# Performance work log

Hardware: AMD Instinct MI355X
Metric: run time of the kernel (lower is better)

## Reference

```python
import jax, jax.numpy as jnp
import numpy as np

K = 20           # neighbors
ALPHA = 1.0      # clustering alpha
BN_EPS = 1e-5
NEG_SLOPE = 0.2


def knn_idx(x, k):
    # x: (B, C, N) -> idx (B, N, k) of k nearest neighbors by squared L2
    xx = jnp.sum(x * x, axis=1)                      # (B, N)
    inner = jnp.einsum('bcn,bcm->bnm', x, x)         # (B, N, N)
    pd = -xx[:, :, None] + 2.0 * inner - xx[:, None, :]  # negative sq dist
    return jax.lax.top_k(pd, k)[1]


def graph_feature(x, k):
    # x: (B, C, N) -> (B, 2C, N, k): concat(neighbor - center, center)
    xt = jnp.transpose(x, (0, 2, 1))                 # (B, N, C)
    idx = knn_idx(x, k)                              # (B, N, k)
    feat = jax.vmap(lambda f, i: f[i])(xt, idx)      # (B, N, k, C)
    center = jnp.broadcast_to(xt[:, :, None, :], feat.shape)
    out = jnp.concatenate([feat - center, center], axis=-1)
    return jnp.transpose(out, (0, 3, 1, 2))


def batchnorm(x, g, b, axes):
    # training-mode BN: batch statistics over `axes`, channel axis = 1
    m = jnp.mean(x, axes, keepdims=True)
    v = jnp.var(x, axes, keepdims=True)
    shape = [1] * x.ndim
    shape[1] = x.shape[1]
    return (x - m) / jnp.sqrt(v + BN_EPS) * g.reshape(shape) + b.reshape(shape)


def conv_block2d(x, w, g, b):
    # 1x1 Conv2d (no bias) + BN2d + LeakyReLU; x (B,Cin,N,k), w (Cout,Cin)
    y = jnp.einsum('oc,bcnk->bonk', w, x)
    return jax.nn.leaky_relu(batchnorm(y, g, b, (0, 2, 3)), NEG_SLOPE)


def setup_inputs() -> dict:
    key = jax.random.key(0)
    ks = jax.random.split(key, 16)
    B, C, N = 4, 3, 2048
    d = {
        'x1': jax.random.normal(ks[0], (B, C, N), jnp.float32),
        'x2': jax.random.normal(ks[1], (B, C, N), jnp.float32),
        'w1': jax.random.normal(ks[2], (64, 6), jnp.float32) * 0.1,
        'g1': jnp.ones((64,), jnp.float32), 'b1': jnp.zeros((64,), jnp.float32),
        'w2': jax.random.normal(ks[3], (64, 128), jnp.float32) * 0.1,
        'g2': jnp.ones((64,), jnp.float32), 'b2': jnp.zeros((64,), jnp.float32),
        'w3': jax.random.normal(ks[4], (128, 128), jnp.float32) * 0.1,
        'g3': jnp.ones((128,), jnp.float32), 'b3': jnp.zeros((128,), jnp.float32),
        'w4': jax.random.normal(ks[5], (256, 256), jnp.float32) * 0.1,
        'g4': jnp.ones((256,), jnp.float32), 'b4': jnp.zeros((256,), jnp.float32),
        'w5': jax.random.normal(ks[6], (1024, 512), jnp.float32) * 0.05,
        'g5': jnp.ones((1024,), jnp.float32), 'b5': jnp.zeros((1024,), jnp.float32),
        'lw1': jax.random.normal(ks[7], (256, 2048), jnp.float32) * 0.02,
        'lb1': jnp.zeros((256,), jnp.float32),
        'lw2': jax.random.normal(ks[8], (64, 256), jnp.float32) * 0.05,
        'lb2': jnp.zeros((64,), jnp.float32),
        'lw3': jax.random.normal(ks[9], (10, 64), jnp.float32) * 0.1,
        'lb3': jnp.zeros((10,), jnp.float32),
        'cw': jax.random.normal(ks[10], (800, 10), jnp.float32) * 0.1,
    }
    return d


def reference(x1, x2, w1, g1, b1, w2, g2, b2, w3, g3, b3, w4, g4, b4,
              w5, g5, b5, lw1, lb1, lw2, lb2, lw3, lb3, cw):

    def single(x):
        h = conv_block2d(graph_feature(x, K), w1, g1, b1)
        f1 = h.max(axis=-1)                            # (B,64,N)
        h = conv_block2d(graph_feature(f1, K), w2, g2, b2)
        f2 = h.max(axis=-1)                            # (B,64,N)
        h = conv_block2d(graph_feature(f2, K), w3, g3, b3)
        f3 = h.max(axis=-1)                            # (B,128,N)
        h = conv_block2d(graph_feature(f3, K), w4, g4, b4)
        f4 = h.max(axis=-1)                            # (B,256,N)
        h = jnp.concatenate([f1, f2, f3, f4], axis=1)  # (B,512,N)
        h = jnp.einsum('oc,bcn->bon', w5, h)           # 1x1 Conv1d
        h = jax.nn.leaky_relu(batchnorm(h, g5, b5, (0, 2)), NEG_SLOPE)
        z = jnp.concatenate([h.max(axis=-1), h.mean(axis=-1)], axis=1)  # (B,2048)
        z = z @ lw1.T + lb1
        z = z @ lw2.T + lb2
        e = z @ lw3.T + lb3                            # (B,10)
        diff = e[:, None, :] - cw                      # (B,800,10)
        x_dis = jnp.sum(diff * diff, axis=2)           # (B,800)
        q = (1.0 + x_dis / ALPHA) ** (-(ALPHA + 1.0) / 2.0)
        q = q / jnp.sum(q, axis=1, keepdims=True)
        return q, e, x_dis

    q1, e1, xd1 = single(x1)
    q2, e2, xd2 = single(x2)
    d = e1 - e2 + 1e-6  # torch F.pairwise_distance eps
    sim = jnp.sqrt(jnp.sum(d * d, axis=1))
    return (sim, q1, q2, e1, e2, xd1)
```

## Files before the change

kernel.cpp:

```cpp
#include <hip/hip_runtime.h>
#include <math.h>

#define BB 4
#define NN 2048
#define KK 20
#define NEG 0.2f

#define QOFF0 4
#define QOFF1 3204
#define EOFF0 6404
#define EOFF1 6444
#define XDOFF 6484

typedef unsigned short u16;
typedef unsigned int u32;
typedef __attribute__((ext_vector_type(8))) short s16x8;
typedef __attribute__((ext_vector_type(16))) float f32x16;
typedef __attribute__((ext_vector_type(8))) u16 u16x8;

__global__ __launch_bounds__(256) void transpose_x_kernel(
    const float* __restrict__ x, float* __restrict__ fnc, float* __restrict__ xx)
{
    int gid = blockIdx.x * 256 + threadIdx.x;
    int b = gid >> 11, n = gid & 2047;
    float s = 0.f;
#pragma unroll
    for (int c = 0; c < 3; ++c) {
        float v = x[((size_t)b * 3 + c) * NN + n];
        fnc[(size_t)gid * 3 + c] = v;
        s += v * v;
    }
    xx[gid] = s;
}

__global__ __launch_bounds__(256) void norms_kernel(
    const float* __restrict__ h512, int choff, int C, float* __restrict__ xx)
{
    int gid = blockIdx.x * 256 + threadIdx.x;
    const float* p = h512 + (size_t)gid * 512 + choff;
    float s = 0.f;
    for (int c = 0; c < C; ++c) { float v = p[c]; s += v * v; }
    xx[gid] = s;
}

#define NINFV -3.4e38f

template<int CTRL>
__device__ __forceinline__ void dmax2(float& a1, float& a2)
{
    int b1i = __builtin_amdgcn_update_dpp(
        __float_as_int(a1), __float_as_int(a1), CTRL, 0xf, 0xf, false);
    int b2i = __builtin_amdgcn_update_dpp(
        __float_as_int(a2), __float_as_int(a2), CTRL, 0xf, 0xf, false);
    float b1 = __int_as_float(b1i), b2 = __int_as_float(b2i);
    float n1 = fmaxf(a1, b1);
    float n2 = fmaxf(fminf(a1, b1), fmaxf(a2, b2));
    a1 = n1; a2 = n2;
}

template<int C>
__global__ __launch_bounds__(512, 4) void knn_kernel(
    const float* __restrict__ fcn,
    const float* __restrict__ fnc,
    int ncs, int choff,
    const float* __restrict__ xx, int* __restrict__ idxout)
{
    __shared__ float sbuf[8][NN];
    int tid = threadIdx.x;
    int bid = blockIdx.x;
    int b   = bid & 3;
    int n0  = (((bid >> 3) << 1) | ((bid >> 2) & 1)) * 8;

    const float* fb = fcn + (size_t)b * C * NN;
    const float* xb = xx + b * NN;
    const float* cbase = fnc + (size_t)(b * NN + n0) * ncs + choff;

    float a0[8], a1[8], a2[8], a3[8];
#pragma unroll
    for (int r = 0; r < 8; ++r) { a0[r] = 0.f; a1[r] = 0.f; a2[r] = 0.f; a3[r] = 0.f; }

    const float* fp = fb + 4 * tid;

    if constexpr (C % 4 == 0) {
        float4 buf[4];
#pragma unroll
        for (int q = 0; q < 4; ++q) buf[q] = *(const float4*)(fp + (size_t)q * NN);
        for (int cg = 0; cg < C; cg += 4) {
            float4 nxt[4];
            if (cg + 4 < C) {
#pragma unroll
                for (int q = 0; q < 4; ++q)
                    nxt[q] = *(const float4*)(fp + (size_t)(cg + 4 + q) * NN);
            } else {
#pragma unroll
                for (int q = 0; q < 4; ++q) nxt[q] = buf[q];
            }
            float4 cv[8];
#pragma unroll
            for (int r = 0; r < 8; ++r)
                cv[r] = *(const float4*)(cbase + (size_t)r * ncs + cg);
#pragma unroll
            for (int r = 0; r < 8; ++r) {
                a0[r] += cv[r].x * buf[0].x; a1[r] += cv[r].x * buf[0].y;
                a2[r] += cv[r].x * buf[0].z; a3[r] += cv[r].x * buf[0].w;
                a0[r] += cv[r].y * buf[1].x; a1[r] += cv[r].y * buf[1].y;
                a2[r] += cv[r].y * buf[1].z; a3[r] += cv[r].y * buf[1].w;
                a0[r] += cv[r].z * buf[2].x; a1[r] += cv[r].z * buf[2].y;
                a2[r] += cv[r].z * buf[2].z; a3[r] += cv[r].z * buf[2].w;
                a0[r] += cv[r].w * buf[3].x; a1[r] += cv[r].w * buf[3].y;
                a2[r] += cv[r].w * buf[3].z; a3[r] += cv[r].w * buf[3].w;
            }
#pragma unroll
            for (int q = 0; q < 4; ++q) buf[q] = nxt[q];
        }
    } else {
        for (int c = 0; c < C; ++c) {
            float cr[8];
#pragma unroll
            for (int r = 0; r < 8; ++r) cr[r] = cbase[(size_t)r * ncs + c];
            float4 v = *(const float4*)(fp + (size_t)c * NN);
#pragma unroll
            for (int r = 0; r < 8; ++r) {
                a0[r] += cr[r] * v.x; a1[r] += cr[r] * v.y;
                a2[r] += cr[r] * v.z; a3[r] += cr[r] * v.w;
            }
        }
    }
    {
        float4 xm = *(const float4*)(xb + 4 * tid);
#pragma unroll
        for (int r = 0; r < 8; ++r) {
            float4 sv = {2.f * a0[r] - xm.x, 2.f * a1[r] - xm.y,
                         2.f * a2[r] - xm.z, 2.f * a3[r] - xm.w};
            *(float4*)&sbuf[r][4 * tid] = sv;
        }
    }
    __syncthreads();

    int w = tid >> 6, lane = tid & 63;
    float* sb = sbuf[w];
    int p = n0 + w;
    int* op = idxout + (size_t)(b * NN + p) * KK;

    if (lane == 0) op[0] = p;
    if (lane == (p & 63)) sb[p] = NINFV;

    float v1 = NINFV, v2 = NINFV, v3 = NINFV, v4 = NINFV;
    int j1 = -1, j2 = -1, j3 = -1, j4 = -1;
#pragma unroll
    for (int j = 0; j < 32; ++j) {
        float vv = sb[lane + (j << 6)];
        if (vv > v1) { v4 = v3; j4 = j3; v3 = v2; j3 = j2; v2 = v1; j2 = j1; v1 = vv; j1 = j; }
        else if (vv > v2) { v4 = v3; j4 = j3; v3 = v2; j3 = j2; v2 = vv; j2 = j; }
        else if (vv > v3) { v4 = v3; j4 = j3; v3 = vv; j3 = j; }
        else if (vv > v4) { v4 = vv; j4 = j; }
    }

    unsigned consumed = 0u;

    for (int it = 1; it < KK; it += 2) {
        float r1 = v1, r2 = v2;
        dmax2<0x111>(r1, r2);
        dmax2<0x112>(r1, r2);
        dmax2<0x114>(r1, r2);
        dmax2<0x118>(r1, r2);
        dmax2<0x142>(r1, r2);
        dmax2<0x143>(r1, r2);
        float m1 = __int_as_float(
            __builtin_amdgcn_readlane(__float_as_int(r1), 63));
        float m2 = __int_as_float(
            __builtin_amdgcn_readlane(__float_as_int(r2), 63));
        unsigned long long k1 = __ballot(v1 == m1);
        if (lane == __ffsll(k1) - 1) {
            op[it] = lane + (j1 << 6);
            consumed |= 1u << j1;
            v1 = v2; j1 = j2; v2 = v3; j2 = j3; v3 = v4; j3 = j4;
            v4 = NINFV; j4 = -1;
        }
        if (it + 1 < KK) {
            unsigned long long k2 = __ballot(v1 == m2);
            if (lane == __ffsll(k2) - 1) {
                op[it + 1] = lane + (j1 << 6);
                consumed |= 1u << j1;
                v1 = v2; j1 = j2; v2 = v3; j2 = j3; v3 = v4; j3 = j4;
                v4 = NINFV; j4 = -1;
            }
        }
        if (__any(v2 == NINFV)) {
            if (v2 == NINFV) {
                v1 = NINFV; v2 = NINFV; v3 = NINFV; v4 = NINFV;
                j1 = -1; j2 = -1; j3 = -1; j4 = -1;
#pragma unroll
                for (int j = 0; j < 32; ++j) {
                    if (!(consumed & (1u << j))) {
                        float vv = sb[lane + (j << 6)];
                        if (vv > v1) { v4 = v3; j4 = j3; v3 = v2; j3 = j2; v2 = v1; j2 = j1; v1 = vv; j1 = j; }
                        else if (vv > v2) { v4 = v3; j4 = j3; v3 = v2; j3 = j2; v2 = vv; j2 = j; }
                        else if (vv > v3) { v4 = v3; j4 = j3; v3 = vv; j3 = j; }
                        else if (vv > v4) { v4 = vv; j4 = j; }
                    }
                }
            }
        }
    }
}

template<int C, int COUT>
__global__ __launch_bounds__(256) void gemm_gh_kernel(
    const float* __restrict__ fnc, int ncs, int choff,
    const float* __restrict__ W,
    float* __restrict__ G, float* __restrict__ H)
{
    constexpr int GROUPS = 256 / COUT;
    constexpr int RPT = 8 / GROUPS;
    __shared__ float Fs[8][C];
    int tid = threadIdx.x;
    int row0 = blockIdx.x * 8;
    for (int i = tid; i < 8 * C; i += 256) {
        int r = i / C, c = i % C;
        Fs[r][c] = fnc[(size_t)(row0 + r) * ncs + choff + c];
    }
    __syncthreads();
    int o = tid % COUT;
    int r0 = (tid / COUT) * RPT;
    float g[RPT], h[RPT];
#pragma unroll
    for (int r = 0; r < RPT; ++r) { g[r] = 0.f; h[r] = 0.f; }
    const float* wr = W + (size_t)o * 2 * C;
    for (int c = 0; c < C; ++c) {
        float w1 = wr[c], wd = wr[C + c] - w1;
#pragma unroll
        for (int r = 0; r < RPT; ++r) {
            float f = Fs[r0 + r][c];
            g[r] += f * w1; h[r] += f * wd;
        }
    }
#pragma unroll
    for (int r = 0; r < RPT; ++r) {
        size_t rr = (size_t)(row0 + r0 + r) * COUT + o;
        G[rr] = g[r]; H[rr] = h[r];
    }
}

template<int COUT>
__global__ __launch_bounds__(256) void gather_kernel(
    const float* __restrict__ G, const float* __restrict__ H,
    const int* __restrict__ idx,
    float* __restrict__ ymax, float* __restrict__ ymin,
    float* __restrict__ psum, float* __restrict__ psumsq)
{
    constexpr int RPI = 256 / COUT;
    constexpr int NITER = 16 / RPI;
    int tid = threadIdx.x;
    int o = tid % COUT;
    int rsub = tid / COUT;
    int row0 = blockIdx.x * 16;
    float s = 0.f, s2 = 0.f;
    for (int it = 0; it < NITER; ++it) {
        int r = row0 + it * RPI + rsub;
        int b = r >> 11;
        float h = H[(size_t)r * COUT + o];
        const int* ip = idx + (size_t)r * KK;
        float mx = -3.4e38f, mn = 3.4e38f;
#pragma unroll
        for (int j = 0; j < KK; ++j) {
            int m = ip[j];
            float g = G[((size_t)(b << 11) + m) * COUT + o];
            float y = g + h;
            mx = fmaxf(mx, y); mn = fminf(mn, y);
            s += y; s2 += y * y;
        }
        ymax[(size_t)r * COUT + o] = mx;
        ymin[(size_t)r * COUT + o] = mn;
    }
    __shared__ float ls[256], ls2[256];
    ls[tid] = s; ls2[tid] = s2;
    __syncthreads();
    for (int st = 128; st >= COUT; st >>= 1) {
        if (tid < st) { ls[tid] += ls[tid + st]; ls2[tid] += ls2[tid + st]; }
        __syncthreads();
    }
    if (tid < COUT) {
        psum[(size_t)blockIdx.x * COUT + tid]   = ls[tid];
        psumsq[(size_t)blockIdx.x * COUT + tid] = ls2[tid];
    }
}

__global__ __launch_bounds__(256) void bnscale_kernel(
    const float* __restrict__ psum, const float* __restrict__ psumsq,
    int nblk, int cout, float cnt,
    const float* __restrict__ gw, const float* __restrict__ bw,
    float* __restrict__ ss)
{
    int o = blockIdx.x;
    int t = threadIdx.x;
    float s = 0.f, s2 = 0.f;
    for (int i = t; i < nblk; i += 256) {
        s  += psum[(size_t)i * cout + o];
        s2 += psumsq[(size_t)i * cout + o];
    }
    __shared__ float ls[256], ls2[256];
    ls[t] = s; ls2[t] = s2;
    __syncthreads();
    for (int st = 128; st > 0; st >>= 1) {
        if (t < st) { ls[t] += ls[t + st]; ls2[t] += ls2[t + st]; }
        __syncthreads();
    }
    if (t == 0) {
        float m = ls[0] / cnt;
        float v = ls2[0] / cnt - m * m;
        float sc = gw[o] / sqrtf(v + 1e-5f);
        float sh = bw[o] - m * sc;
        ss[o * 2] = sc; ss[o * 2 + 1] = sh;
    }
}

__global__ __launch_bounds__(256) void apply_kernel(
    const float* __restrict__ ymax, const float* __restrict__ ymin,
    const float* __restrict__ ss, int coutShift, int choff,
    float* __restrict__ h512)
{
    size_t gid = (size_t)blockIdx.x * 256 + threadIdx.x;
    int o = (int)(gid & ((1u << coutShift) - 1));
    size_t r = gid >> coutShift;
    float sc = ss[o * 2], sh = ss[o * 2 + 1];
    float v = (sc >= 0.f) ? ymax[gid] : ymin[gid];
    float a = sc * v + sh;
    float act = (a > 0.f) ? a : NEG * a;
    h512[r * 512 + choff + o] = act;
}

template<int CO>
__global__ __launch_bounds__(256) void apply_t_kernel(
    const float* __restrict__ ymax, const float* __restrict__ ymin,
    const float* __restrict__ ss, int choff,
    float* __restrict__ h512, float* __restrict__ fcn)
{
    constexpr int TILES_O = CO >> 6;
    __shared__ float tile[64][65];
    int tr = blockIdx.x / TILES_O;
    int to = blockIdx.x % TILES_O;
    int r0 = tr * 64, o0 = to * 64;
    int t = threadIdx.x;
    int lr = t >> 6;
    int lo = t & 63;
    int o = o0 + lo;
    float sc = ss[o * 2], sh = ss[o * 2 + 1];
#pragma unroll
    for (int rr = 0; rr < 64; rr += 4) {
        int r = r0 + rr + lr;
        size_t gid = (size_t)r * CO + o;
        float v = (sc >= 0.f) ? ymax[gid] : ymin[gid];
        float a = sc * v + sh;
        float act = (a > 0.f) ? a : NEG * a;
        h512[(size_t)r * 512 + choff + o] = act;
        tile[rr + lr][lo] = act;
    }
    __syncthreads();
    int b = r0 >> 11;
    int n0 = r0 & 2047;
#pragma unroll
    for (int oo = 0; oo < 64; oo += 4) {
        fcn[((size_t)(b * CO + o0 + oo + lr)) * NN + n0 + lo] = tile[lo][oo + lr];
    }
}

__device__ __forceinline__ u16 f2bf(float x) {
    u32 u = __float_as_uint(x);
    u += 0x7FFFu + ((u >> 16) & 1u);
    return (u16)(u >> 16);
}

__global__ __launch_bounds__(256) void tobf16_kernel(
    const float* __restrict__ A, const float* __restrict__ Bm,
    u16* __restrict__ Ah, u16* __restrict__ Al,
    u16* __restrict__ Bh, u16* __restrict__ Bl)
{
    int gid = blockIdx.x * 256 + threadIdx.x;
    const float* src; u16 *dh, *dl; size_t off;
    if (gid < 524288) { src = A;  dh = Ah; dl = Al; off = (size_t)gid * 8; }
    else             { src = Bm; dh = Bh; dl = Bl; off = (size_t)(gid - 524288) * 8; }
    float4 v0 = *(const float4*)(src + off);
    float4 v1 = *(const float4*)(src + off + 4);
    float x[8] = {v0.x, v0.y, v0.z, v0.w, v1.x, v1.y, v1.z, v1.w};
    u16x8 h, l;
#pragma unroll
    for (int j = 0; j < 8; ++j) {
        u16 hb = f2bf(x[j]);
        h[j] = hb;
        l[j] = f2bf(x[j] - __uint_as_float((u32)hb << 16));
    }
    *(u16x8*)(dh + off) = h;
    *(u16x8*)(dl + off) = l;
}

__device__ __forceinline__ void gload_lds16(const void* g, void* l) {
    __builtin_amdgcn_global_load_lds(
        (const __attribute__((address_space(1))) void*)g,
        (__attribute__((address_space(3))) void*)l, 16, 0, 0);
}

__global__ __launch_bounds__(256) void gemm5_mfma_kernel(
    const u16* __restrict__ Ah, const u16* __restrict__ Al,
    const u16* __restrict__ Bh, const u16* __restrict__ Bl,
    float* __restrict__ Y, float* __restrict__ psum, float* __restrict__ psumsq)
{
    __shared__ u16 As[2][128][64];
    __shared__ u16 Bs[2][128][64];
    __shared__ float scs[4][128];
    __shared__ float sqs[4][128];

    int tid = threadIdx.x;
    int bm = blockIdx.x & 63, bn = blockIdx.x >> 6;
    int row0 = bm * 128, col0 = bn * 128;
    int w = tid >> 6, lane = tid & 63;
    int wr = w >> 1, wc = w & 1;

    int isB = w >> 1, plane = w & 1;
    int srow = lane >> 3;
    int kch  = (lane & 7) ^ srow;
    const u16* gbase = isB ? (plane ? Bl : Bh) : (plane ? Al : Ah);
    int rc0 = isB ? col0 : row0;
    const u16* gsrc0 = gbase + (size_t)(rc0 + srow) * 512 + kch * 8;
    u16* lds0 = (isB ? &Bs[0][0][0] : &As[0][0][0]) + plane * 8192;

    f32x16 acc[2][2];
#pragma unroll
    for (int i = 0; i < 2; ++i)
#pragma unroll
        for (int j = 0; j < 2; ++j)
#pragma unroll
            for (int r = 0; r < 16; ++r) acc[i][j][r] = 0.f;

    int ln = lane & 31, l5 = lane >> 5;
    const u16* Afb = &As[0][0][0] + (size_t)(wr * 64 + ln) * 64;
    const u16* Bfb = &Bs[0][0][0] + (size_t)(wc * 64 + ln) * 64;

    for (int k0 = 0; k0 < 512; k0 += 64) {
#pragma unroll
        for (int cc = 0; cc < 16; ++cc)
            gload_lds16(gsrc0 + (size_t)cc * 4096 + k0, lds0 + cc * 512);
        __syncthreads();

#pragma unroll
        for (int ks = 0; ks < 4; ++ks) {
            int pos = ((ks * 2 + l5) ^ (ln & 7)) * 8;
            s16x8 ah0 = *(const s16x8*)(Afb + pos);
            s16x8 ah1 = *(const s16x8*)(Afb + 2048 + pos);
            s16x8 al0 = *(const s16x8*)(Afb + 8192 + pos);
            s16x8 al1 = *(const s16x8*)(Afb + 8192 + 2048 + pos);
#pragma unroll
            for (int j = 0; j < 2; ++j) {
                s16x8 bh = *(const s16x8*)(Bfb + j * 2048 + pos);
                s16x8 bl = *(const s16x8*)(Bfb + 8192 + j * 2048 + pos);
                acc[0][j] = __builtin_amdgcn_mfma_f32_32x32x16_bf16(ah0, bh, acc[0][j], 0, 0, 0);
                acc[1][j] = __builtin_amdgcn_mfma_f32_32x32x16_bf16(ah1, bh, acc[1][j], 0, 0, 0);
                acc[0][j] = __builtin_amdgcn_mfma_f32_32x32x16_bf16(al0, bh, acc[0][j], 0, 0, 0);
                acc[1][j] = __builtin_amdgcn_mfma_f32_32x32x16_bf16(al1, bh, acc[1][j], 0, 0, 0);
                acc[0][j] = __builtin_amdgcn_mfma_f32_32x32x16_bf16(ah0, bl, acc[0][j], 0, 0, 0);
                acc[1][j] = __builtin_amdgcn_mfma_f32_32x32x16_bf16(ah1, bl, acc[1][j], 0, 0, 0);
            }
        }
        __syncthreads();
    }

#pragma unroll
    for (int i = 0; i < 2; ++i)
#pragma unroll
        for (int reg = 0; reg < 16; ++reg) {
            int row = row0 + wr * 64 + i * 32 + l5 * 4 + (reg >> 2) * 8 + (reg & 3);
            float* yp = Y + (size_t)row * 1024 + col0 + wc * 64 + ln;
            yp[0]  = acc[i][0][reg];
            yp[32] = acc[i][1][reg];
        }

#pragma unroll
// ... 137 lines not shown
#pragma unroll
        for (int i = 0; i < 10; ++i) { float d = es[b][i] - cwr[i]; xd += d * d; }
        qs[p] = 1.0f / (1.0f + xd);
        if (which == 0) out[XDOFF + p] = xd;
    }
    __syncthreads();
    if (t < 4) {
        float s = 0.f;
        for (int j = 0; j < 800; ++j) s += qs[t * 800 + j];
        dnm[t] = s;
    }
    __syncthreads();
    int qoff = (which == 0) ? QOFF0 : QOFF1;
    for (int p = t; p < 3200; p += 1024) out[qoff + p] = qs[p] / dnm[p / 800];
}

__global__ void sim_kernel(const float* __restrict__ e_store, float* __restrict__ out)
{
    int t = threadIdx.x;
    if (t < 4) {
        float s = 0.f;
        for (int i = 0; i < 10; ++i) {
            float d = e_store[t * 10 + i] - e_store[40 + t * 10 + i] + 1e-6f;
            s += d * d;
        }
        out[t] = sqrtf(s);
    }
}

extern "C" void kernel_launch(void* const* d_in, const int* in_sizes, int n_in,
                              void* d_out, int out_size, void* d_ws, size_t ws_size,
                              hipStream_t stream)
{
    const float* x1  = (const float*)d_in[0];
    const float* x2  = (const float*)d_in[1];
    const float* w1  = (const float*)d_in[2];
    const float* g1  = (const float*)d_in[3];
    const float* b1  = (const float*)d_in[4];
    const float* w2  = (const float*)d_in[5];
    const float* g2  = (const float*)d_in[6];
    const float* b2  = (const float*)d_in[7];
    const float* w3  = (const float*)d_in[8];
    const float* g3  = (const float*)d_in[9];
    const float* b3  = (const float*)d_in[10];
    const float* w4  = (const float*)d_in[11];
    const float* g4  = (const float*)d_in[12];
    const float* b4  = (const float*)d_in[13];
    const float* w5  = (const float*)d_in[14];
    const float* g5  = (const float*)d_in[15];
    const float* b5  = (const float*)d_in[16];
    const float* lw1 = (const float*)d_in[17];
    const float* lb1 = (const float*)d_in[18];
    const float* lw2 = (const float*)d_in[19];
    const float* lb2 = (const float*)d_in[20];
    const float* lw3 = (const float*)d_in[21];
    const float* lb3 = (const float*)d_in[22];
    const float* cw  = (const float*)d_in[23];
    float* out = (float*)d_out;

    float* ws   = (float*)d_ws;
    float* h512 = ws;
    float* G    = h512 + 4194304;
    float* Hb   = G + 2097152;
    float* ymax = Hb + 2097152;
    float* ymin = ymax + 2097152;
    float* y5   = G;
    float* fcn  = ymin + 2097152;
    float* fnc1 = fcn + 1048576;
    float* xx   = fnc1 + 32768;
    float* psum = xx + 8192;
    float* psq  = psum + 131072;
    float* ss   = psq + 131072;
    float* p5s  = ss + 2048;
    float* p5q  = p5s + 262144;
    float* ss5  = p5q + 262144;
    float* z    = ss5 + 2048;
    float* z1   = z + 8192;
    float* est  = z1 + 1024;
    int*   idx  = (int*)(est + 128);
    u16*   Ahs  = (u16*)(idx + BB * NN * KK);
    u16*   Als  = Ahs + 4194304;
    u16*   Bhs  = Als + 4194304;
    u16*   Bls  = Bhs + 524288;

    for (int which = 0; which < 2; ++which) {
        const float* xin = which ? x2 : x1;
        transpose_x_kernel<<<32, 256, 0, stream>>>(xin, fnc1, xx);
        knn_kernel<3><<<1024, 512, 0, stream>>>(xin, fnc1, 3, 0, xx, idx);
        gemm_gh_kernel<3, 64><<<1024, 256, 0, stream>>>(fnc1, 3, 0, w1, G, Hb);
        gather_kernel<64><<<512, 256, 0, stream>>>(G, Hb, idx, ymax, ymin, psum, psq);
        bnscale_kernel<<<64, 256, 0, stream>>>(psum, psq, 512, 64, 163840.f, g1, b1, ss);
        apply_t_kernel<64><<<128, 256, 0, stream>>>(ymax, ymin, ss, 0, h512, fcn);
        norms_kernel<<<32, 256, 0, stream>>>(h512, 0, 64, xx);
        knn_kernel<64><<<1024, 512, 0, stream>>>(fcn, h512, 512, 0, xx, idx);
        gemm_gh_kernel<64, 64><<<1024, 256, 0, stream>>>(h512, 512, 0, w2, G, Hb);
        gather_kernel<64><<<512, 256, 0, stream>>>(G, Hb, idx, ymax, ymin, psum, psq);
        bnscale_kernel<<<64, 256, 0, stream>>>(psum, psq, 512, 64, 163840.f, g2, b2, ss);
        apply_t_kernel<64><<<128, 256, 0, stream>>>(ymax, ymin, ss, 64, h512, fcn);
        norms_kernel<<<32, 256, 0, stream>>>(h512, 64, 64, xx);
        knn_kernel<64><<<1024, 512, 0, stream>>>(fcn, h512, 512, 64, xx, idx);
        gemm_gh_kernel<64, 128><<<1024, 256, 0, stream>>>(h512, 512, 64, w3, G, Hb);
        gather_kernel<128><<<512, 256, 0, stream>>>(G, Hb, idx, ymax, ymin, psum, psq);
        bnscale_kernel<<<128, 256, 0, stream>>>(psum, psq, 512, 128, 163840.f, g3, b3, ss);
        apply_t_kernel<128><<<256, 256, 0, stream>>>(ymax, ymin, ss, 128, h512, fcn);
        norms_kernel<<<32, 256, 0, stream>>>(h512, 128, 128, xx);
        knn_kernel<128><<<1024, 512, 0, stream>>>(fcn, h512, 512, 128, xx, idx);
        gemm_gh_kernel<128, 256><<<1024, 256, 0, stream>>>(h512, 512, 128, w4, G, Hb);
        gather_kernel<256><<<512, 256, 0, stream>>>(G, Hb, idx, ymax, ymin, psum, psq);
        bnscale_kernel<<<256, 256, 0, stream>>>(psum, psq, 512, 256, 163840.f, g4, b4, ss);
        apply_kernel<<<8192, 256, 0, stream>>>(ymax, ymin, ss, 8, 256, h512);
        tobf16_kernel<<<2304, 256, 0, stream>>>(h512, w5, Ahs, Als, Bhs, Bls);
        gemm5_mfma_kernel<<<512, 256, 0, stream>>>(Ahs, Als, Bhs, Bls, y5, p5s, p5q);
        bnscale_kernel<<<1024, 256, 0, stream>>>(p5s, p5q, 64, 1024, 8192.f, g5, b5, ss5);
        pool_part_kernel<<<256, 256, 0, stream>>>(y5, ss5, p5s, p5q);
        pool_comb_kernel<<<4, 256, 0, stream>>>(p5s, p5q, z);
        gemv1_kernel<<<256, 64, 0, stream>>>(z, lw1, lb1, z1);
        head2_kernel<<<1, 1024, 0, stream>>>(z1, lw2, lb2, lw3, lb3, cw, out, est, which);
    }
    sim_kernel<<<1, 64, 0, stream>>>(est, out);
}
```

Baseline: 1.170 ms.

## Compute kNN distance matrix with split-bf16 MFMA and fuse bf16 conversion into apply

Replaces the FP32 CUDA-core inner-product loop in the kNN kernel with 16x16x32 bf16 MFMA using a hi/lo split (three products) to approximate FP32 accuracy, processing 16 query points per 1024-thread block. The bf16 hi/lo copies of activations are now written directly by the apply kernels and by the input transpose (zero-padded to 32 channels), and the standalone tobf16 pass for the activations is removed. The weight conversion is hoisted out of the per-input loop. This adds extra stores in the apply kernels and risks small distance errors that could change neighbor selection on near ties.

Measured after the change: 1.239 ms. 1.06x slower.

```diff
diff --git a/kernel.cpp b/kernel.cpp
--- a/kernel.cpp
+++ b/kernel.cpp
@@ -15,22 +15,45 @@
 typedef unsigned short u16;
 typedef unsigned int u32;
 typedef __attribute__((ext_vector_type(8))) short s16x8;
+typedef __attribute__((ext_vector_type(4))) float f32x4;
 typedef __attribute__((ext_vector_type(16))) float f32x16;
 typedef __attribute__((ext_vector_type(8))) u16 u16x8;
 
+__device__ __forceinline__ u16 f2bf(float x) {
+    u32 u = __float_as_uint(x);
+    u += 0x7FFFu + ((u >> 16) & 1u);
+    return (u16)(u >> 16);
+}
+
 __global__ __launch_bounds__(256) void transpose_x_kernel(
-    const float* __restrict__ x, float* __restrict__ fnc, float* __restrict__ xx)
+    const float* __restrict__ x, float* __restrict__ fnc, float* __restrict__ xx,
+    u16* __restrict__ fh, u16* __restrict__ fl)
 {
     int gid = blockIdx.x * 256 + threadIdx.x;
     int b = gid >> 11, n = gid & 2047;
     float s = 0.f;
+    float v[3];
 #pragma unroll
     for (int c = 0; c < 3; ++c) {
-        float v = x[((size_t)b * 3 + c) * NN + n];
-        fnc[(size_t)gid * 3 + c] = v;
-        s += v * v;
+        v[c] = x[((size_t)b * 3 + c) * NN + n];
+        fnc[(size_t)gid * 3 + c] = v[c];
+        s += v[c] * v[c];
     }
     xx[gid] = s;
+    u16x8 z = {0,0,0,0,0,0,0,0};
+    u16x8 h0 = z, l0 = z;
+#pragma unroll
+    for (int c = 0; c < 3; ++c) {
+        u16 hb = f2bf(v[c]);
+        h0[c] = hb;
+        l0[c] = f2bf(v[c] - __uint_as_float((u32)hb << 16));
+    }
+    u16* fhp = fh + (size_t)gid * 32;
+    u16* flp = fl + (size_t)gid * 32;
+    *(u16x8*)(fhp)      = h0; *(u16x8*)(fhp + 8)  = z;
+    *(u16x8*)(fhp + 16) = z;  *(u16x8*)(fhp + 24) = z;
+    *(u16x8*)(flp)      = l0; *(u16x8*)(flp + 8)  = z;
+    *(u16x8*)(flp + 16) = z;  *(u16x8*)(flp + 24) = z;
 }
 
 __global__ __launch_bounds__(256) void norms_kernel(
@@ -58,88 +81,57 @@
     a1 = n1; a2 = n2;
 }
 
-template<int C>
-__global__ __launch_bounds__(512, 4) void knn_kernel(
-    const float* __restrict__ fcn,
-    const float* __restrict__ fnc,
+template<int KT>
+__global__ __launch_bounds__(1024, 4) void knn_mfma_kernel(
+    const u16* __restrict__ Fh, const u16* __restrict__ Fl,
     int ncs, int choff,
     const float* __restrict__ xx, int* __restrict__ idxout)
 {
-    __shared__ float sbuf[8][NN];
+    __shared__ float sbuf[16][NN];
     int tid = threadIdx.x;
     int bid = blockIdx.x;
     int b   = bid & 3;
-    int n0  = (((bid >> 3) << 1) | ((bid >> 2) & 1)) * 8;
-
-    const float* fb = fcn + (size_t)b * C * NN;
+    int n0  = (bid >> 2) << 4;
+    int wv = tid >> 6, lane = tid & 63;
+    int l15 = lane & 15, l4 = lane >> 4;
+
+    const u16* Ahp = Fh + (size_t)(b * NN + n0 + l15) * ncs + choff + l4 * 8;
+    const u16* Alp = Fl + (size_t)(b * NN + n0 + l15) * ncs + choff + l4 * 8;
+    s16x8 a_h[KT], a_l[KT];
+#pragma unroll
+    for (int kt = 0; kt < KT; ++kt) {
+        a_h[kt] = *(const s16x8*)(Ahp + kt * 32);
+        a_l[kt] = *(const s16x8*)(Alp + kt * 32);
+    }
+
     const float* xb = xx + b * NN;
-    const float* cbase = fnc + (size_t)(b * NN + n0) * ncs + choff;
-
-    float a0[8], a1[8], a2[8], a3[8];
-#pragma unroll
-    for (int r = 0; r < 8; ++r) { a0[r] = 0.f; a1[r] = 0.f; a2[r] = 0.f; a3[r] = 0.f; }
-
-    const float* fp = fb + 4 * tid;
-
-    if constexpr (C % 4 == 0) {
-        float4 buf[4];
-#pragma unroll
-        for (int q = 0; q < 4; ++q) buf[q] = *(const float4*)(fp + (size_t)q * NN);
-        for (int cg = 0; cg < C; cg += 4) {
-            float4 nxt[4];
-            if (cg + 4 < C) {
-#pragma unroll
-                for (int q = 0; q < 4; ++q)
-                    nxt[q] = *(const float4*)(fp + (size_t)(cg + 4 + q) * NN);
-            } else {
-#pragma unroll
-                for (int q = 0; q < 4; ++q) nxt[q] = buf[q];
-            }
-            float4 cv[8];
-#pragma unroll
-            for (int r = 0; r < 8; ++r)
-                cv[r] = *(const float4*)(cbase + (size_t)r * ncs + cg);
-#pragma unroll
-            for (int r = 0; r < 8; ++r) {
-                a0[r] += cv[r].x * buf[0].x; a1[r] += cv[r].x * buf[0].y;
-                a2[r] += cv[r].x * buf[0].z; a3[r] += cv[r].x * buf[0].w;
-                a0[r] += cv[r].y * buf[1].x; a1[r] += cv[r].y * buf[1].y;
-                a2[r] += cv[r].y * buf[1].z; a3[r] += cv[r].y * buf[1].w;
-                a0[r] += cv[r].z * buf[2].x; a1[r] += cv[r].z * buf[2].y;
-                a2[r] += cv[r].z * buf[2].z; a3[r] += cv[r].z * buf[2].w;
-                a0[r] += cv[r].w * buf[3].x; a1[r] += cv[r].w * buf[3].y;
-                a2[r] += cv[r].w * buf[3].z; a3[r] += cv[r].w * buf[3].w;
-            }
-#pragma unroll
-            for (int q = 0; q < 4; ++q) buf[q] = nxt[q];
-        }
-    } else {
-        for (int c = 0; c < C; ++c) {
-            float cr[8];
-#pragma unroll
-            for (int r = 0; r < 8; ++r) cr[r] = cbase[(size_t)r * ncs + c];
-            float4 v = *(const float4*)(fp + (size_t)c * NN);
-#pragma unroll
-            for (int r = 0; r < 8; ++r) {
-                a0[r] += cr[r] * v.x; a1[r] += cr[r] * v.y;
-                a2[r] += cr[r] * v.z; a3[r] += cr[r] * v.w;
-            }
-        }
-    }
-    {
-        float4 xm = *(const float4*)(xb + 4 * tid);
-#pragma unroll
-        for (int r = 0; r < 8; ++r) {
-            float4 sv = {2.f * a0[r] - xm.x, 2.f * a1[r] - xm.y,
-                         2.f * a2[r] - xm.z, 2.f * a3[r] - xm.w};
-            *(float4*)&sbuf[r][4 * tid] = sv;
-        }
-    }
-    __syncthreads();
-
-    int w = tid >> 6, lane = tid & 63;
-    float* sb = sbuf[w];
-    int p = n0 + w;
+#pragma unroll
+    for (int ct = 0; ct < 8; ++ct) {
+        int m0 = (wv << 7) + (ct << 4);
+        const u16* Bhp = Fh + (size_t)(b * NN + m0 + l15) * ncs + choff + l4 * 8;
+        const u16* Blp = Fl + (size_t)(b * NN + m0 + l15) * ncs + choff + l4 * 8;
+        f32x4 acc;
+#pragma unroll
+        for (int i = 0; i < 4; ++i) acc[i] = 0.f;
+#pragma unroll
+        for (int kt = 0; kt < KT; ++kt) {
+            s16x8 bh = *(const s16x8*)(Bhp + kt * 32);
+            s16x8 bl = *(const s16x8*)(Blp + kt * 32);
+            acc = __builtin_amdgcn_mfma_f32_16x16x32_bf16(a_h[kt], bh, acc, 0, 0, 0);
+            acc = __builtin_amdgcn_mfma_f32_16x16x32_bf16(a_l[kt], bh, acc, 0, 0, 0);
+            acc = __builtin_amdgcn_mfma_f32_16x16x32_bf16(a_h[kt], bl, acc, 0, 0, 0);
+        }
+        float xv = xb[m0 + l15];
+#pragma unroll
+        for (int i = 0; i < 4; ++i) {
+            int row = l4 * 4 + i;
+            sbuf[row][m0 + l15] = 2.f * acc[i] - xv;
+        }
+    }
+    __syncthreads();
+
+    float* sb = sbuf[wv];
+    int p = n0 + wv;
     int* op = idxout + (size_t)(b * NN + p) * KK;
 
     if (lane == 0) op[0] = p;
@@ -318,7 +310,7 @@
 __global__ __launch_bounds__(256) void apply_kernel(
     const float* __restrict__ ymax, const float* __restrict__ ymin,
     const float* __restrict__ ss, int coutShift, int choff,
-    float* __restrict__ h512)
+    float* __restrict__ h512, u16* __restrict__ Ah, u16* __restrict__ Al)
 {
     size_t gid = (size_t)blockIdx.x * 256 + threadIdx.x;
     int o = (int)(gid & ((1u << coutShift) - 1));
@@ -327,14 +319,19 @@
     float v = (sc >= 0.f) ? ymax[gid] : ymin[gid];
     float a = sc * v + sh;
     float act = (a > 0.f) ? a : NEG * a;
-    h512[r * 512 + choff + o] = act;
+    size_t hidx = r * 512 + choff + o;
+    h512[hidx] = act;
+    u16 hb = f2bf(act);
+    Ah[hidx] = hb;
+    Al[hidx] = f2bf(act - __uint_as_float((u32)hb << 16));
 }
 
 template<int CO>
 __global__ __launch_bounds__(256) void apply_t_kernel(
     const float* __restrict__ ymax, const float* __restrict__ ymin,
     const float* __restrict__ ss, int choff,
-    float* __restrict__ h512, float* __restrict__ fcn)
+    float* __restrict__ h512, float* __restrict__ fcn,
+    u16* __restrict__ Ah, u16* __restrict__ Al)
 {
     constexpr int TILES_O = CO >> 6;
     __shared__ float tile[64][65];
@@ -353,7 +350,11 @@
         float v = (sc >= 0.f) ? ymax[gid] : ymin[gid];
         float a = sc * v + sh;
         float act = (a > 0.f) ? a : NEG * a;
-        h512[(size_t)r * 512 + choff + o] = act;
+        size_t hidx = (size_t)r * 512 + choff + o;
+        h512[hidx] = act;
+        u16 hb = f2bf(act);
+        Ah[hidx] = hb;
+        Al[hidx] = f2bf(act - __uint_as_float((u32)hb << 16));
         tile[rr + lr][lo] = act;
     }
     __syncthreads();
@@ -365,23 +366,13 @@
     }
 }
 
-__device__ __forceinline__ u16 f2bf(float x) {
-    u32 u = __float_as_uint(x);
-    u += 0x7FFFu + ((u >> 16) & 1u);
-    return (u16)(u >> 16);
-}
-
-__global__ __launch_bounds__(256) void tobf16_kernel(
-    const float* __restrict__ A, const float* __restrict__ Bm,
-    u16* __restrict__ Ah, u16* __restrict__ Al,
-    u16* __restrict__ Bh, u16* __restrict__ Bl)
+__global__ __launch_bounds__(256) void tobf16_b_kernel(
+    const float* __restrict__ Bm, u16* __restrict__ Bh, u16* __restrict__ Bl)
 {
     int gid = blockIdx.x * 256 + threadIdx.x;
-    const float* src; u16 *dh, *dl; size_t off;
-    if (gid < 524288) { src = A;  dh = Ah; dl = Al; off = (size_t)gid * 8; }
-    else             { src = Bm; dh = Bh; dl = Bl; off = (size_t)(gid - 524288) * 8; }
-    float4 v0 = *(const float4*)(src + off);
-    float4 v1 = *(const float4*)(src + off + 4);
+    size_t off = (size_t)gid * 8;
+    float4 v0 = *(const float4*)(Bm + off);
+    float4 v1 = *(const float4*)(Bm + off + 4);
     float x[8] = {v0.x, v0.y, v0.z, v0.w, v1.x, v1.y, v1.z, v1.w};
     u16x8 h, l;
 #pragma unroll
@@ -390,8 +381,8 @@
         h[j] = hb;
         l[j] = f2bf(x[j] - __uint_as_float((u32)hb << 16));
     }
-    *(u16x8*)(dh + off) = h;
-    *(u16x8*)(dl + off) = l;
+    *(u16x8*)(Bh + off) = h;
+    *(u16x8*)(Bl + off) = l;
 }
 
 __device__ __forceinline__ void gload_lds16(const void* g, void* l) {
@@ -695,34 +686,37 @@
     u16*   Als  = Ahs + 4194304;
     u16*   Bhs  = Als + 4194304;
     u16*   Bls  = Bhs + 524288;
+    u16*   fnc1h = Bls + 524288;
+    u16*   fnc1l = fnc1h + 262144;
+
+    tobf16_b_kernel<<<256, 256, 0, stream>>>(w5, Bhs, Bls);
 
     for (int which = 0; which < 2; ++which) {
         const float* xin = which ? x2 : x1;
-        transpose_x_kernel<<<32, 256, 0, stream>>>(xin, fnc1, xx);
-        knn_kernel<3><<<1024, 512, 0, stream>>>(xin, fnc1, 3, 0, xx, idx);
+        transpose_x_kernel<<<32, 256, 0, stream>>>(xin, fnc1, xx, fnc1h, fnc1l);
+        knn_mfma_kernel<1><<<512, 1024, 0, stream>>>(fnc1h, fnc1l, 32, 0, xx, idx);
         gemm_gh_kernel<3, 64><<<1024, 256, 0, stream>>>(fnc1, 3, 0, w1, G, Hb);
         gather_kernel<64><<<512, 256, 0, stream>>>(G, Hb, idx, ymax, ymin, psum, psq);
         bnscale_kernel<<<64, 256, 0, stream>>>(psum, psq, 512, 64, 163840.f, g1, b1, ss);
-        apply_t_kernel<64><<<128, 256, 0, stream>>>(ymax, ymin, ss, 0, h512, fcn);
+        apply_t_kernel<64><<<128, 256, 0, stream>>>(ymax, ymin, ss, 0, h512, fcn, Ahs, Als);
         norms_kernel<<<32, 256, 0, stream>>>(h512, 0, 64, xx);
-        knn_kernel<64><<<1024, 512, 0, stream>>>(fcn, h512, 512, 0, xx, idx);
+        knn_mfma_kernel<2><<<512, 1024, 0, stream>>>(Ahs, Als, 512, 0, xx, idx);
         gemm_gh_kernel<64, 64><<<1024, 256, 0, stream>>>(h512, 512, 0, w2, G, Hb);
         gather_kernel<64><<<512, 256, 0, stream>>>(G, Hb, idx, ymax, ymin, psum, psq);
         bnscale_kernel<<<64, 256, 0, stream>>>(psum, psq, 512, 64, 163840.f, g2, b2, ss);
-        apply_t_kernel<64><<<128, 256, 0, stream>>>(ymax, ymin, ss, 64, h512, fcn);
+        apply_t_kernel<64><<<128, 256, 0, stream>>>(ymax, ymin, ss, 64, h512, fcn, Ahs, Als);
         norms_kernel<<<32, 256, 0, stream>>>(h512, 64, 64, xx);
-        knn_kernel<64><<<1024, 512, 0, stream>>>(fcn, h512, 512, 64, xx, idx);
+        knn_mfma_kernel<2><<<512, 1024, 0, stream>>>(Ahs, Als, 512, 64, xx, idx);
         gemm_gh_kernel<64, 128><<<1024, 256, 0, stream>>>(h512, 512, 64, w3, G, Hb);
         gather_kernel<128><<<512, 256, 0, stream>>>(G, Hb, idx, ymax, ymin, psum, psq);
         bnscale_kernel<<<128, 256, 0, stream>>>(psum, psq, 512, 128, 163840.f, g3, b3, ss);
-        apply_t_kernel<128><<<256, 256, 0, stream>>>(ymax, ymin, ss, 128, h512, fcn);
+        apply_t_kernel<128><<<256, 256, 0, stream>>>(ymax, ymin, ss, 128, h512, fcn, Ahs, Als);
         norms_kernel<<<32, 256, 0, stream>>>(h512, 128, 128, xx);
-        knn_kernel<128><<<1024, 512, 0, stream>>>(fcn, h512, 512, 128, xx, idx);
+        knn_mfma_kernel<4><<<512, 1024, 0, stream>>>(Ahs, Als, 512, 128, xx, idx);
         gemm_gh_kernel<128, 256><<<1024, 256, 0, stream>>>(h512, 512, 128, w4, G, Hb);
         gather_kernel<256><<<512, 256, 0, stream>>>(G, Hb, idx, ymax, ymin, psum, psq);
         bnscale_kernel<<<256, 256, 0, stream>>>(psum, psq, 512, 256, 163840.f, g4, b4, ss);
-        apply_kernel<<<8192, 256, 0, stream>>>(ymax, ymin, ss, 8, 256, h512);
-        tobf16_kernel<<<2304, 256, 0, stream>>>(h512, w5, Ahs, Als, Bhs, Bls);
+        apply_kernel<<<8192, 256, 0, stream>>>(ymax, ymin, ss, 8, 256, h512, Ahs, Als);
         gemm5_mfma_kernel<<<512, 256, 0, stream>>>(Ahs, Als, Bhs, Bls, y5, p5s, p5q);
         bnscale_kernel<<<1024, 256, 0, stream>>>(p5s, p5q, 64, 1024, 8192.f, g5, b5, ss5);
         pool_part_kernel<<<256, 256, 0, stream>>>(y5, ss5, p5s, p5q);
```

## Move edge-conv G/H GEMMs to split-bf16 MFMA and fuse bf16 conversion into producers

Applied to the files above, without the earlier changes.

Replaces the scalar fp32 per-point GEMM that computes the G and H projections with a 16x16x32 bf16 MFMA kernel. It uses a hi/lo split (three MFMAs per k-step) to keep near-fp32 accuracy. The bf16 hi/lo copies of activations are now written directly by the apply kernels and the input transpose, so the separate activation conversion pass before the final GEMM is dropped. Weight conversion to bf16 is done once up front. This trades extra MFMA work and larger bf16 writes in the apply kernels for removing the slow FMA GEMMs and one full conversion pass.

Measured after the change: 1.086 ms, median of 2. 1.08x faster.

```diff
diff --git a/kernel.cpp b/kernel.cpp
--- a/kernel.cpp
+++ b/kernel.cpp
@@ -15,22 +15,45 @@
 typedef unsigned short u16;
 typedef unsigned int u32;
 typedef __attribute__((ext_vector_type(8))) short s16x8;
+typedef __attribute__((ext_vector_type(4))) float f32x4;
 typedef __attribute__((ext_vector_type(16))) float f32x16;
 typedef __attribute__((ext_vector_type(8))) u16 u16x8;
 
+__device__ __forceinline__ u16 f2bf(float x) {
+    u32 u = __float_as_uint(x);
+    u += 0x7FFFu + ((u >> 16) & 1u);
+    return (u16)(u >> 16);
+}
+
 __global__ __launch_bounds__(256) void transpose_x_kernel(
-    const float* __restrict__ x, float* __restrict__ fnc, float* __restrict__ xx)
+    const float* __restrict__ x, float* __restrict__ fnc, float* __restrict__ xx,
+    u16* __restrict__ fh, u16* __restrict__ fl)
 {
     int gid = blockIdx.x * 256 + threadIdx.x;
     int b = gid >> 11, n = gid & 2047;
     float s = 0.f;
+    float v[3];
 #pragma unroll
     for (int c = 0; c < 3; ++c) {
-        float v = x[((size_t)b * 3 + c) * NN + n];
-        fnc[(size_t)gid * 3 + c] = v;
-        s += v * v;
+        v[c] = x[((size_t)b * 3 + c) * NN + n];
+        fnc[(size_t)gid * 3 + c] = v[c];
+        s += v[c] * v[c];
     }
     xx[gid] = s;
+    u16x8 z = {0,0,0,0,0,0,0,0};
+    u16x8 h0 = z, l0 = z;
+#pragma unroll
+    for (int c = 0; c < 3; ++c) {
+        u16 hb = f2bf(v[c]);
+        h0[c] = hb;
+        l0[c] = f2bf(v[c] - __uint_as_float((u32)hb << 16));
+    }
+    u16* fhp = fh + (size_t)gid * 32;
+    u16* flp = fl + (size_t)gid * 32;
+    *(u16x8*)(fhp)      = h0; *(u16x8*)(fhp + 8)  = z;
+    *(u16x8*)(fhp + 16) = z;  *(u16x8*)(fhp + 24) = z;
+    *(u16x8*)(flp)      = l0; *(u16x8*)(flp + 8)  = z;
+    *(u16x8*)(flp + 16) = z;  *(u16x8*)(flp + 24) = z;
 }
 
 __global__ __launch_bounds__(256) void norms_kernel(
@@ -205,40 +228,68 @@
     }
 }
 
-template<int C, int COUT>
-__global__ __launch_bounds__(256) void gemm_gh_kernel(
-    const float* __restrict__ fnc, int ncs, int choff,
-    const float* __restrict__ W,
+__global__ __launch_bounds__(256) void tobf16_w_kernel(
+    const float* __restrict__ W, int C, int COUT, int KP,
+    u16* __restrict__ Wh, u16* __restrict__ Wl)
+{
+    int idx = blockIdx.x * 256 + threadIdx.x;
+    if (idx >= 2 * COUT * KP) return;
+    int row = idx / KP, c = idx - row * KP;
+    int o = (row >= COUT) ? row - COUT : row;
+    float val = 0.f;
+    if (c < C) {
+        float w1 = W[(size_t)o * 2 * C + c];
+        val = (row >= COUT) ? (W[(size_t)o * 2 * C + C + c] - w1) : w1;
+    }
+    u16 hb = f2bf(val);
+    Wh[idx] = hb;
+    Wl[idx] = f2bf(val - __uint_as_float((u32)hb << 16));
+}
+
+template<int KT, int COUT>
+__global__ __launch_bounds__(256) void gemm_gh_mfma_kernel(
+    const u16* __restrict__ Fh, const u16* __restrict__ Fl,
+    int ncs, int choff,
+    const u16* __restrict__ Wh, const u16* __restrict__ Wl,
     float* __restrict__ G, float* __restrict__ H)
 {
-    constexpr int GROUPS = 256 / COUT;
-    constexpr int RPT = 8 / GROUPS;
-    __shared__ float Fs[8][C];
+    constexpr int KP = KT * 32;
+    constexpr int NT = (2 * COUT) >> 4;
     int tid = threadIdx.x;
-    int row0 = blockIdx.x * 8;
-    for (int i = tid; i < 8 * C; i += 256) {
-        int r = i / C, c = i % C;
-        Fs[r][c] = fnc[(size_t)(row0 + r) * ncs + choff + c];
-    }
-    __syncthreads();
-    int o = tid % COUT;
-    int r0 = (tid / COUT) * RPT;
-    float g[RPT], h[RPT];
-#pragma unroll
-    for (int r = 0; r < RPT; ++r) { g[r] = 0.f; h[r] = 0.f; }
-    const float* wr = W + (size_t)o * 2 * C;
-    for (int c = 0; c < C; ++c) {
-        float w1 = wr[c], wd = wr[C + c] - w1;
-#pragma unroll
-        for (int r = 0; r < RPT; ++r) {
-            float f = Fs[r0 + r][c];
-            g[r] += f * w1; h[r] += f * wd;
-        }
-    }
-#pragma unroll
-    for (int r = 0; r < RPT; ++r) {
-        size_t rr = (size_t)(row0 + r0 + r) * COUT + o;
-        G[rr] = g[r]; H[rr] = h[r];
+    int r0 = blockIdx.x << 4;
+    int wv = tid >> 6, lane = tid & 63;
+    int l15 = lane & 15, l4 = lane >> 4;
+
+    const u16* Ah0 = Fh + (size_t)(r0 + l15) * ncs + choff + l4 * 8;
+    const u16* Al0 = Fl + (size_t)(r0 + l15) * ncs + choff + l4 * 8;
+    s16x8 a_h[KT], a_l[KT];
+#pragma unroll
+    for (int kt = 0; kt < KT; ++kt) {
+        a_h[kt] = *(const s16x8*)(Ah0 + kt * 32);
+        a_l[kt] = *(const s16x8*)(Al0 + kt * 32);
+    }
+
+    for (int t = wv; t < NT; t += 4) {
+        int c0 = t << 4;
+        const u16* Bh0 = Wh + (size_t)(c0 + l15) * KP + l4 * 8;
+        const u16* Bl0 = Wl + (size_t)(c0 + l15) * KP + l4 * 8;
+        f32x4 acc;
+#pragma unroll
+        for (int i = 0; i < 4; ++i) acc[i] = 0.f;
+#pragma unroll
+        for (int kt = 0; kt < KT; ++kt) {
+            s16x8 bh = *(const s16x8*)(Bh0 + kt * 32);
+            s16x8 bl = *(const s16x8*)(Bl0 + kt * 32);
+            acc = __builtin_amdgcn_mfma_f32_16x16x32_bf16(a_h[kt], bh, acc, 0, 0, 0);
+            acc = __builtin_amdgcn_mfma_f32_16x16x32_bf16(a_l[kt], bh, acc, 0, 0, 0);
+            acc = __builtin_amdgcn_mfma_f32_16x16x32_bf16(a_h[kt], bl, acc, 0, 0, 0);
+        }
+        int col = c0 + l15;
+        float* dst = (col < COUT) ? G : H;
+        int cc = (col < COUT) ? col : col - COUT;
+#pragma unroll
+        for (int i = 0; i < 4; ++i)
+            dst[(size_t)(r0 + l4 * 4 + i) * COUT + cc] = acc[i];
     }
 }
 
@@ -318,7 +369,7 @@
 __global__ __launch_bounds__(256) void apply_kernel(
     const float* __restrict__ ymax, const float* __restrict__ ymin,
     const float* __restrict__ ss, int coutShift, int choff,
-    float* __restrict__ h512)
+    float* __restrict__ h512, u16* __restrict__ Ah, u16* __restrict__ Al)
 {
     size_t gid = (size_t)blockIdx.x * 256 + threadIdx.x;
     int o = (int)(gid & ((1u << coutShift) - 1));
@@ -327,14 +378,19 @@
     float v = (sc >= 0.f) ? ymax[gid] : ymin[gid];
     float a = sc * v + sh;
     float act = (a > 0.f) ? a : NEG * a;
-    h512[r * 512 + choff + o] = act;
+    size_t hidx = r * 512 + choff + o;
+    h512[hidx] = act;
+    u16 hb = f2bf(act);
+    Ah[hidx] = hb;
+    Al[hidx] = f2bf(act - __uint_as_float((u32)hb << 16));
 }
 
 template<int CO>
 __global__ __launch_bounds__(256) void apply_t_kernel(
     const float* __restrict__ ymax, const float* __restrict__ ymin,
     const float* __restrict__ ss, int choff,
-    float* __restrict__ h512, float* __restrict__ fcn)
+    float* __restrict__ h512, float* __restrict__ fcn,
+    u16* __restrict__ Ah, u16* __restrict__ Al)
 {
     constexpr int TILES_O = CO >> 6;
     __shared__ float tile[64][65];
@@ -353,7 +409,11 @@
         float v = (sc >= 0.f) ? ymax[gid] : ymin[gid];
         float a = sc * v + sh;
         float act = (a > 0.f) ? a : NEG * a;
-        h512[(size_t)r * 512 + choff + o] = act;
+        size_t hidx = (size_t)r * 512 + choff + o;
+        h512[hidx] = act;
+        u16 hb = f2bf(act);
+        Ah[hidx] = hb;
+        Al[hidx] = f2bf(act - __uint_as_float((u32)hb << 16));
         tile[rr + lr][lo] = act;
     }
     __syncthreads();
@@ -365,23 +425,13 @@
     }
 }
 
-__device__ __forceinline__ u16 f2bf(float x) {
-    u32 u = __float_as_uint(x);
-    u += 0x7FFFu + ((u >> 16) & 1u);
-    return (u16)(u >> 16);
-}
-
-__global__ __launch_bounds__(256) void tobf16_kernel(
-    const float* __restrict__ A, const float* __restrict__ Bm,
-    u16* __restrict__ Ah, u16* __restrict__ Al,
-    u16* __restrict__ Bh, u16* __restrict__ Bl)
+__global__ __launch_bounds__(256) void tobf16_b_kernel(
+    const float* __restrict__ Bm, u16* __restrict__ Bh, u16* __restrict__ Bl)
 {
     int gid = blockIdx.x * 256 + threadIdx.x;
-    const float* src; u16 *dh, *dl; size_t off;
-    if (gid < 524288) { src = A;  dh = Ah; dl = Al; off = (size_t)gid * 8; }
-    else             { src = Bm; dh = Bh; dl = Bl; off = (size_t)(gid - 524288) * 8; }
-    float4 v0 = *(const float4*)(src + off);
-    float4 v1 = *(const float4*)(src + off + 4);
+    size_t off = (size_t)gid * 8;
+    float4 v0 = *(const float4*)(Bm + off);
+    float4 v1 = *(const float4*)(Bm + off + 4);
     float x[8] = {v0.x, v0.y, v0.z, v0.w, v1.x, v1.y, v1.z, v1.w};
     u16x8 h, l;
 #pragma unroll
@@ -390,8 +440,8 @@
         h[j] = hb;
         l[j] = f2bf(x[j] - __uint_as_float((u32)hb << 16));
     }
-    *(u16x8*)(dh + off) = h;
-    *(u16x8*)(dl + off) = l;
+    *(u16x8*)(Bh + off) = h;
+    *(u16x8*)(Bl + off) = l;
 }
 
 __device__ __forceinline__ void gload_lds16(const void* g, void* l) {
@@ -695,34 +745,43 @@
     u16*   Als  = Ahs + 4194304;
     u16*   Bhs  = Als + 4194304;
     u16*   Bls  = Bhs + 524288;
+    u16*   fnc1h = Bls + 524288;
+    u16*   fnc1l = fnc1h + 262144;
+    u16*   Wh   = fnc1l + 262144;
+    u16*   Wl   = Wh + 98304;
+
+    tobf16_b_kernel<<<256, 256, 0, stream>>>(w5, Bhs, Bls);
+    tobf16_w_kernel<<<16,  256, 0, stream>>>(w1, 3,   64,  32,  Wh,         Wl);
+    tobf16_w_kernel<<<32,  256, 0, stream>>>(w2, 64,  64,  64,  Wh + 4096,  Wl + 4096);
+    tobf16_w_kernel<<<64,  256, 0, stream>>>(w3, 64,  128, 64,  Wh + 12288, Wl + 12288);
+    tobf16_w_kernel<<<256, 256, 0, stream>>>(w4, 128, 256, 128, Wh + 28672, Wl + 28672);
 
     for (int which = 0; which < 2; ++which) {
         const float* xin = which ? x2 : x1;
-        transpose_x_kernel<<<32, 256, 0, stream>>>(xin, fnc1, xx);
+        transpose_x_kernel<<<32, 256, 0, stream>>>(xin, fnc1, xx, fnc1h, fnc1l);
         knn_kernel<3><<<1024, 512, 0, stream>>>(xin, fnc1, 3, 0, xx, idx);
-        gemm_gh_kernel<3, 64><<<1024, 256, 0, stream>>>(fnc1, 3, 0, w1, G, Hb);
+        gemm_gh_mfma_kernel<1, 64><<<512, 256, 0, stream>>>(fnc1h, fnc1l, 32, 0, Wh, Wl, G, Hb);
         gather_kernel<64><<<512, 256, 0, stream>>>(G, Hb, idx, ymax, ymin, psum, psq);
         bnscale_kernel<<<64, 256, 0, stream>>>(psum, psq, 512, 64, 163840.f, g1, b1, ss);
-        apply_t_kernel<64><<<128, 256, 0, stream>>>(ymax, ymin, ss, 0, h512, fcn);
+        apply_t_kernel<64><<<128, 256, 0, stream>>>(ymax, ymin, ss, 0, h512, fcn, Ahs, Als);
         norms_kernel<<<32, 256, 0, stream>>>(h512, 0, 64, xx);
         knn_kernel<64><<<1024, 512, 0, stream>>>(fcn, h512, 512, 0, xx, idx);
-        gemm_gh_kernel<64, 64><<<1024, 256, 0, stream>>>(h512, 512, 0, w2, G, Hb);
+        gemm_gh_mfma_kernel<2, 64><<<512, 256, 0, stream>>>(Ahs, Als, 512, 0, Wh + 4096, Wl + 4096, G, Hb);
         gather_kernel<64><<<512, 256, 0, stream>>>(G, Hb, idx, ymax, ymin, psum, psq);
         bnscale_kernel<<<64, 256, 0, stream>>>(psum, psq, 512, 64, 163840.f, g2, b2, ss);
-        apply_t_kernel<64><<<128, 256, 0, stream>>>(ymax, ymin, ss, 64, h512, fcn);
+        apply_t_kernel<64><<<128, 256, 0, stream>>>(ymax, ymin, ss, 64, h512, fcn, Ahs, Als);
         norms_kernel<<<32, 256, 0, stream>>>(h512, 64, 64, xx);
         knn_kernel<64><<<1024, 512, 0, stream>>>(fcn, h512, 512, 64, xx, idx);
-        gemm_gh_kernel<64, 128><<<1024, 256, 0, stream>>>(h512, 512, 64, w3, G, Hb);
+        gemm_gh_mfma_kernel<2, 128><<<512, 256, 0, stream>>>(Ahs, Als, 512, 64, Wh + 12288, Wl + 12288, G, Hb);
         gather_kernel<128><<<512, 256, 0, stream>>>(G, Hb, idx, ymax, ymin, psum, psq);
         bnscale_kernel<<<128, 256, 0, stream>>>(psum, psq, 512, 128, 163840.f, g3, b3, ss);
-        apply_t_kernel<128><<<256, 256, 0, stream>>>(ymax, ymin, ss, 128, h512, fcn);
+        apply_t_kernel<128><<<256, 256, 0, stream>>>(ymax, ymin, ss, 128, h512, fcn, Ahs, Als);
         norms_kernel<<<32, 256, 0, stream>>>(h512, 128, 128, xx);
         knn_kernel<128><<<1024, 512, 0, stream>>>(fcn, h512, 512, 128, xx, idx);
-        gemm_gh_kernel<128, 256><<<1024, 256, 0, stream>>>(h512, 512, 128, w4, G, Hb);
+        gemm_gh_mfma_kernel<4, 256><<<512, 256, 0, stream>>>(Ahs, Als, 512, 128, Wh + 28672, Wl + 28672, G, Hb);
         gather_kernel<256><<<512, 256, 0, stream>>>(G, Hb, idx, ymax, ymin, psum, psq);
         bnscale_kernel<<<256, 256, 0, stream>>>(psum, psq, 512, 256, 163840.f, g4, b4, ss);
-        apply_kernel<<<8192, 256, 0, stream>>>(ymax, ymin, ss, 8, 256, h512);
-        tobf16_kernel<<<2304, 256, 0, stream>>>(h512, w5, Ahs, Als, Bhs, Bls);
+        apply_kernel<<<8192, 256, 0, stream>>>(ymax, ymin, ss, 8, 256, h512, Ahs, Als);
         gemm5_mfma_kernel<<<512, 256, 0, stream>>>(Ahs, Als, Bhs, Bls, y5, p5s, p5q);
         bnscale_kernel<<<1024, 256, 0, stream>>>(p5s, p5q, 64, 1024, 8192.f, g5, b5, ss5);
         pool_part_kernel<<<256, 256, 0, stream>>>(y5, ss5, p5s, p5q);
```
